# Kernel optimization log

Measured on AMD Instinct MI355X. Metric: run time of the kernel, lower is better.

The kernel has to match this reference:

```python
import jax, jax.numpy as jnp
import numpy as np

EPS = 1e-8
N_NODES = 100000
N_EDGES = 3200000
S_IN, V_IN = 128, 16
S_OUT, V_OUT = 128, 16
HID = 16          # bottleneck=1 -> max(V_IN, V_OUT)
FRAME_C = 3       # scalarization_vectorization_output_dim
MERGED = HID + S_IN + FRAME_C * 3  # 153


def safe_norm(x, axis):
    return jnp.sqrt(jnp.sum(x * x, axis=axis) + EPS)


def setup_inputs() -> dict:
    key = jax.random.key(0)
    ks = jax.random.split(key, 12)
    scalar_rep = jax.random.normal(ks[0], (N_NODES, S_IN), dtype=jnp.float32)
    vector_rep = jax.random.normal(ks[1], (N_NODES, V_IN, 3), dtype=jnp.float32)
    frames = jax.random.normal(ks[2], (N_EDGES, 3, 3), dtype=jnp.float32)
    edge_index = jax.random.randint(ks[3], (2, N_EDGES), 0, N_NODES, dtype=jnp.int64)
    s = 0.05
    W_down = jax.random.normal(ks[4], (HID, V_IN), dtype=jnp.float32) * s
    W_frames = jax.random.normal(ks[5], (FRAME_C, V_IN), dtype=jnp.float32) * s
    W_scalar = jax.random.normal(ks[6], (S_OUT, MERGED), dtype=jnp.float32) * s
    b_scalar = jnp.zeros((S_OUT,), dtype=jnp.float32)
    W_up = jax.random.normal(ks[7], (V_OUT, HID), dtype=jnp.float32) * s
    W_gate = jax.random.normal(ks[8], (V_OUT, S_OUT), dtype=jnp.float32) * s
    b_gate = jnp.zeros((V_OUT,), dtype=jnp.float32)
    return {"scalar_rep": scalar_rep, "vector_rep": vector_rep, "frames": frames,
            "W_down": W_down, "W_frames": W_frames, "W_scalar": W_scalar,
            "b_scalar": b_scalar, "W_up": W_up, "W_gate": W_gate, "b_gate": b_gate,
            "edge_index": edge_index}


def reference(scalar_rep, vector_rep, frames, W_down, W_frames, W_scalar,
              b_scalar, W_up, W_gate, b_gate, edge_index):
    N = scalar_rep.shape[0]
    row = edge_index[0]
    # vector branch: [N, V, 3] -> [N, 3, V]
    v_pre = jnp.swapaxes(vector_rep, -1, -2)
    vh = jnp.einsum('ntv,hv->nth', v_pre, W_down)          # [N, 3, H]
    vnorm = safe_norm(vh, axis=-2)                          # [N, H]
    vdf = jnp.einsum('ntv,fv->ntf', v_pre, W_frames)        # [N, 3, F=3]
    # scalarize: gather per-edge, frame matmul over spatial dim, scatter-mean
    m = jnp.einsum('est,etf->esf', frames, vdf[row])        # [E, 3(s), 3(f)]
    local = jnp.swapaxes(m, -1, -2).reshape(m.shape[0], 9)  # [E, 9] (f, s) order
    sums = jax.ops.segment_sum(local, row, num_segments=N)
    cnt = jax.ops.segment_sum(jnp.ones((local.shape[0],), dtype=local.dtype),
                              row, num_segments=N)
    scalar_hidden = sums / jnp.maximum(cnt, 1.0)[:, None]   # [N, 9]
    merged = jnp.concatenate([scalar_rep, vnorm, scalar_hidden], axis=-1)  # [N, 153]
    s_out = merged @ W_scalar.T + b_scalar                  # [N, S_OUT]
    # vectorize with sigmoid gate
    v_up = jnp.einsum('nth,vh->ntv', vh, W_up)              # [N, 3, V_OUT]
    v_rep = jnp.swapaxes(v_up, -1, -2)                       # [N, V_OUT, 3]
    gate = jax.nn.silu(s_out) @ W_gate.T + b_gate            # [N, V_OUT]
    v_final = v_rep * jax.nn.sigmoid(gate)[..., None]
    s_final = jax.nn.silu(s_out)
    return s_final, v_final
```

## Files before the change

kernel.cpp:

```cpp
#include <hip/hip_runtime.h>
#include <hip/hip_bf16.h>
#include <math.h>

#define N_NODES 100000
#define N_EDGES 3200000
#define NB 16
#define EPSV 1e-8f

#define NBUCK 782
#define NCHUNK 1280
#define CHUNK_E 2500

#define CE 256
#define RS 264

typedef __attribute__((ext_vector_type(8))) short short8;
typedef __attribute__((ext_vector_type(4))) float f32x4;

static __device__ __forceinline__ unsigned short f2bf(float x) {
  union { float f; unsigned int u; } c; c.f = x;
  unsigned int r = c.u + 0x7fff + ((c.u >> 16) & 1);
  return (unsigned short)(r >> 16);
}

__global__ __launch_bounds__(256) void hist_kernel(const int* __restrict__ row,
                                                   unsigned short* __restrict__ hist,
                                                   unsigned short* __restrict__ lscan) {
  __shared__ int lh[NBUCK];
  __shared__ int wtot[4];
  for (int i = threadIdx.x; i < NBUCK; i += 256) lh[i] = 0;
  __syncthreads();
  const int c = blockIdx.x;
  const int e1 = c * CHUNK_E + CHUNK_E;
  for (int e = c * CHUNK_E + threadIdx.x; e < e1; e += 256)
    atomicAdd(&lh[row[e] >> 7], 1);
  __syncthreads();
  const int t = threadIdx.x, lane = t & 63, wid = t >> 6;
  const int b0 = t * 4;
  int h[4];
#pragma unroll
  for (int j = 0; j < 4; ++j) h[j] = (b0 + j < NBUCK) ? lh[b0 + j] : 0;
  int s = h[0] + h[1] + h[2] + h[3];
  int incl = s;
#pragma unroll
  for (int d = 1; d < 64; d <<= 1) {
    int o = __shfl_up(incl, d);
    if (lane >= d) incl += o;
  }
  if (lane == 63) wtot[wid] = incl;
  __syncthreads();
  int pre = incl - s;
  for (int w = 0; w < wid; ++w) pre += wtot[w];
#pragma unroll
  for (int j = 0; j < 4; ++j) {
    if (b0 + j < NBUCK) {
      hist [(size_t)c * NBUCK + b0 + j] = (unsigned short)h[j];
      lscan[(size_t)c * NBUCK + b0 + j] = (unsigned short)pre;
    }
    pre += h[j];
  }
}

__global__ __launch_bounds__(256) void scanc_kernel(const unsigned short* __restrict__ hist,
                                                    unsigned short* __restrict__ cscan,
                                                    int* __restrict__ total) {
  __shared__ int s[2][NCHUNK];
  const int b = blockIdx.x;
  const int t = threadIdx.x;
  for (int i = t; i < NCHUNK; i += 256) s[0][i] = hist[(size_t)i * NBUCK + b];
  __syncthreads();
  int src = 0;
  for (int off = 1; off < NCHUNK; off <<= 1) {
    int dst = src ^ 1;
    for (int i = t; i < NCHUNK; i += 256)
      s[dst][i] = s[src][i] + ((i >= off) ? s[src][i - off] : 0);
    __syncthreads();
    src = dst;
  }
  for (int i = t; i < NCHUNK; i += 256)
    cscan[(size_t)i * NBUCK + b] = (unsigned short)((i == 0) ? 0 : s[src][i - 1]);
  if (t == 0) total[b] = s[src][NCHUNK - 1];
}

__global__ __launch_bounds__(256) void scanb_kernel(const int* __restrict__ total,
                                                    int* __restrict__ base) {
  __shared__ int s[2][1024];
  const int t = threadIdx.x;
  for (int i = t; i < 1024; i += 256) s[0][i] = (i < NBUCK) ? total[i] : 0;
  __syncthreads();
  int src = 0;
  for (int off = 1; off < 1024; off <<= 1) {
    int dst = src ^ 1;
    for (int i = t; i < 1024; i += 256)
      s[dst][i] = s[src][i] + ((i >= off) ? s[src][i - off] : 0);
    __syncthreads();
    src = dst;
  }
  for (int i = t; i <= NBUCK; i += 256) base[i] = (i == 0) ? 0 : s[src][i - 1];
}

__global__ __launch_bounds__(512) void scatter_kernel(const int* __restrict__ row,
                                                      const unsigned short* __restrict__ lscan,
                                                      const unsigned short* __restrict__ cscan,
                                                      const int* __restrict__ base,
                                                      const float* __restrict__ frames,
                                                      unsigned int* __restrict__ payload) {
  __shared__ unsigned int sbuf[CHUNK_E * 5];
  __shared__ int lstart[NBUCK], loff[NBUCK], runG[NBUCK];
  const int c = blockIdx.x, tid = threadIdx.x;

  for (int i = tid; i < NBUCK; i += 512) {
    int st = (int)lscan[(size_t)c * NBUCK + i];
    lstart[i] = st;
    loff[i] = st;
    runG[i] = base[i] + (int)cscan[(size_t)c * NBUCK + i];
  }
  __syncthreads();

  const int e0 = c * CHUNK_E;
  for (int e = e0 + tid; e < e0 + CHUNK_E; e += 512) {
    int r = row[e];
    const float* f = frames + (size_t)e * 9;
    unsigned int w0 = f2bf(f[0]) | ((unsigned)f2bf(f[1]) << 16);
    unsigned int w1 = f2bf(f[2]) | ((unsigned)f2bf(f[3]) << 16);
    unsigned int w2 = f2bf(f[4]) | ((unsigned)f2bf(f[5]) << 16);
    unsigned int w3 = f2bf(f[6]) | ((unsigned)f2bf(f[7]) << 16);
    unsigned int w4 = f2bf(f[8]) | ((unsigned)(r & 127) << 16);
    int p = atomicAdd(&loff[r >> 7], 1);
    unsigned int* d = sbuf + p * 5;
    d[0] = w0; d[1] = w1; d[2] = w2; d[3] = w3; d[4] = w4;
  }
  __syncthreads();

  const int grp = tid >> 4, gl = tid & 15;
  for (int b = grp; b < NBUCK; b += 32) {
    int ls = lstart[b] * 5;
    int n5 = (loff[b] - lstart[b]) * 5;
    size_t gs = (size_t)runG[b] * 5;
    for (int d = gl; d < n5; d += 16)
      payload[gs + d] = sbuf[ls + d];
  }
}

__global__ __launch_bounds__(256) void reduce_kernel(const unsigned int* __restrict__ payload,
                                                     const int* __restrict__ base,
                                                     float* __restrict__ acc) {
  __shared__ unsigned short stg[2][16][RS];
  const int tid = threadIdx.x;
  const int b = blockIdx.x;
  const int wid = tid >> 6, lane = tid & 63;
  const int lr = lane & 15, lk = lane >> 4;

  for (int i = tid; i < RS; i += 256) {
    stg[0][9][i] = 0x3F80; stg[1][9][i] = 0x3F80;
  }

  const int p0 = base[b], p1 = base[b + 1];
  const int nch = (p1 - p0 + CE - 1) / CE;
  const int s0 = wid * 2;
  const unsigned na = (unsigned)((s0 << 4) | lr);
  const unsigned nbod = (unsigned)(((s0 + 1) << 4) | lr);

  f32x4 c0 = {0.f, 0.f, 0.f, 0.f};
  f32x4 c1 = {0.f, 0.f, 0.f, 0.f};

  auto STAGE = [&](int c, int buf) {
    int p = p0 + c * CE + tid;
    if (p < p1) {
      const unsigned int* s = payload + (size_t)p * 5;
      unsigned int w0 = s[0], w1 = s[1], w2 = s[2], w3 = s[3], w4 = s[4];
      stg[buf][0][tid] = (unsigned short)w0;
      stg[buf][1][tid] = (unsigned short)(w0 >> 16);
      stg[buf][2][tid] = (unsigned short)w1;
      stg[buf][3][tid] = (unsigned short)(w1 >> 16);
      stg[buf][4][tid] = (unsigned short)w2;
      stg[buf][5][tid] = (unsigned short)(w2 >> 16);
      stg[buf][6][tid] = (unsigned short)w3;
      stg[buf][7][tid] = (unsigned short)(w3 >> 16);
      stg[buf][8][tid] = (unsigned short)w4;
      stg[buf][10][tid] = (unsigned short)(w4 >> 16);
    } else {
#pragma unroll
      for (int k = 0; k < 9; ++k) stg[buf][k][tid] = 0;
      stg[buf][10][tid] = 0xFFFF;
    }
  };

  auto COMP = [&](int buf) {
#pragma unroll
    for (int g = 0; g < 8; ++g) {
      short8 bf = *(const short8*)&stg[buf][lr][g * 32 + lk * 8];
      short8 nv = *(const short8*)&stg[buf][10][g * 32 + lk * 8];
      short8 a0, a1;
#pragma unroll
      for (int j = 0; j < 8; ++j) {
        unsigned nid = (unsigned short)nv[j];
        a0[j] = (short)((nid == na)   ? 0x3F80 : 0);
        a1[j] = (short)((nid == nbod) ? 0x3F80 : 0);
      }
      c0 = __builtin_amdgcn_mfma_f32_16x16x32_bf16(a0, bf, c0, 0, 0, 0);
      c1 = __builtin_amdgcn_mfma_f32_16x16x32_bf16(a1, bf, c1, 0, 0, 0);
    }
  };

  if (nch > 0) {
    STAGE(0, 0);
    __syncthreads();
    for (int c = 0; c < nch; ++c) {
      if (c + 1 < nch) STAGE(c + 1, (c + 1) & 1);
      COMP(c & 1);
      __syncthreads();
    }
  }
  const int n0 = b << 7;
  if (lr < 10) {
#pragma unroll
    for (int j = 0; j < 4; ++j) {
      int r = lk * 4 + j;
      int x0 = n0 + s0 * 16 + r;
      int x1 = n0 + (s0 + 1) * 16 + r;
      if (x0 < N_NODES) acc[(size_t)x0 * 10 + lr] = c0[j];
      if (x1 < N_NODES) acc[(size_t)x1 * 10 + lr] = c1[j];
    }
  }
}

__global__ __launch_bounds__(256) void prep_kernel(const float* __restrict__ Ws,
                                                   const float* __restrict__ Wg,
                                                   unsigned short* __restrict__ wsWs,
                                                   unsigned short* __restrict__ wsWg) {
  int idx = blockIdx.x * 256 + threadIdx.x;
  if (idx < 8 * 5 * 512) {
    int j = idx & 7, l = (idx >> 3) & 63, t = idx >> 9;
    int nt = t / 5, kk = t - nt * 5;
    int o = nt * 16 + (l & 15);
    int m = kk * 32 + ((l >> 4) << 3) + j;
    wsWs[idx] = (m < 153) ? f2bf(Ws[o * 153 + m]) : (unsigned short)0;
  }
  if (idx < 4 * 512) {
    int j = idx & 7, l = (idx >> 3) & 63, kk = idx >> 9;
    int v = l & 15;
    int m = kk * 32 + ((l >> 4) << 3) + j;
    wsWg[idx] = f2bf(Wg[v * 128 + m]);
  }
}

__global__ __launch_bounds__(256, 4) void node_kernel(
    const float* __restrict__ scalar_rep,
    const float* __restrict__ vrep,
    const float* __restrict__ Wd,
    const float* __restrict__ Wf,
    const float* __restrict__ bs,
    const float* __restrict__ Wu,
    const float* __restrict__ bg,
    const unsigned short* __restrict__ wsWs,
    const unsigned short* __restrict__ wsWg,
    const float* __restrict__ acc,
    float* __restrict__ out_s,
    float* __restrict__ out_v) {
  __shared__ alignas(16) unsigned short s_mergedb[16 * 168];
  __shared__ alignas(16) unsigned short s_sfb[16 * 136];
  __shared__ float s_vrep[16][48];
  __shared__ float s_vh[16][48];
  __shared__ float s_vdf[16][12];
  __shared__ float s_gate[16][16];
  __shared__ float s_WdT[256], s_WuT[256], s_Wf[48], s_bs[128], s_bg[16];

  const int tid = threadIdx.x;
  {
    int a = tid >> 4, b = tid & 15;
    s_WdT[b * 16 + a] = Wd[tid];
    s_WuT[b * 16 + a] = Wu[tid];
  }
  if (tid < 48) s_Wf[tid] = Wf[tid];
  if (tid < 128) s_bs[tid] = bs[tid];
  if (tid < 16) s_bg[tid] = bg[tid];
  if (tid < 240) {
    int r = tid / 15, c = 153 + tid % 15;
    s_mergedb[r * 168 + c] = 0;
  }

  const int i4 = tid >> 4, j4 = tid & 15;
  const int wid = tid >> 6, lane = tid & 63;
  const int lr = lane & 15, lk = lane >> 4;

  const float4* scalar4 = (const float4*)scalar_rep;
  const float4* vrep4 = (const float4*)vrep;

  for (int g = blockIdx.x; g < N_NODES / NB; g += gridDim.x) {
    const int n0 = g * NB;
    __syncthreads();
    for (int idx = tid; idx < 512; idx += 256) {
      float4 v = scalar4[(size_t)n0 * 32 + idx];
      int r = idx >> 5, c4 = idx & 31;
      unsigned short* d = s_mergedb + r * 168 + c4 * 4;
      d[0] = f2bf(v.x); d[1] = f2bf(v.y); d[2] = f2bf(v.z); d[3] = f2bf(v.w);
    }
    for (int idx = tid; idx < 192; idx += 256)
      ((float4*)s_vrep)[idx] = vrep4[(size_t)n0 * 12 + idx];
    __syncthreads();
    {
      float a0 = 0.f, a1 = 0.f, a2 = 0.f;
#pragma unroll
      for (int v = 0; v < 16; ++v) {
        float w = s_WdT[v * 16 + j4];
        a0 += s_vrep[i4][v * 3 + 0] * w;
        a1 += s_vrep[i4][v * 3 + 1] * w;
        a2 += s_vrep[i4][v * 3 + 2] * w;
      }
      s_vh[i4][j4]      = a0;
      s_vh[i4][16 + j4] = a1;
      s_vh[i4][32 + j4] = a2;
      s_mergedb[i4 * 168 + 128 + j4] = f2bf(sqrtf(a0 * a0 + a1 * a1 + a2 * a2 + EPSV));
    }
    if (j4 < 9) {
      int t = j4 / 3, f = j4 - t * 3;
      float a = 0.f;
#pragma unroll
      for (int v = 0; v < 16; ++v)
        a += s_vrep[i4][v * 3 + t] * s_Wf[f * 16 + v];
      s_vdf[i4][j4] = a;
    }
    __syncthreads();
    if (j4 < 9) {
      int f = j4 / 3, s = j4 - f * 3;
      const float* a = acc + (size_t)(n0 + i4) * 10;
      float c = fmaxf(a[9], 1.0f);
      float sum = a[s * 3 + 0] * s_vdf[i4][0 + f] +
                  a[s * 3 + 1] * s_vdf[i4][3 + f] +
                  a[s * 3 + 2] * s_vdf[i4][6 + f];
      s_mergedb[i4 * 168 + 144 + j4] = f2bf(sum / c);
    }
    __syncthreads();
    {
      const int nt0 = wid * 2;
      short8 afrag[5];
#pragma unroll
      for (int kk = 0; kk < 5; ++kk)
        afrag[kk] = *(const short8*)(s_mergedb + lr * 168 + kk * 32 + lk * 8);
      float b0v = s_bs[nt0 * 16 + lr], b1v = s_bs[nt0 * 16 + 16 + lr];
      f32x4 acc0 = {b0v, b0v, b0v, b0v};
      f32x4 acc1 = {b1v, b1v, b1v, b1v};
#pragma unroll
      for (int kk = 0; kk < 5; ++kk) {
        short8 bf0 = *(const short8*)(wsWs + (((nt0 * 5 + kk) << 6) + lane) * 8);
        short8 bf1 = *(const short8*)(wsWs + ((((nt0 + 1) * 5 + kk) << 6) + lane) * 8);
        acc0 = __builtin_amdgcn_mfma_f32_16x16x32_bf16(afrag[kk], bf0, acc0, 0, 0, 0);
        acc1 = __builtin_amdgcn_mfma_f32_16x16x32_bf16(afrag[kk], bf1, acc1, 0, 0, 0);
      }
#pragma unroll
      for (int j = 0; j < 4; ++j) {
        int node = lk * 4 + j;
        float x0 = acc0[j];
        float sf0 = x0 / (1.0f + __expf(-x0));
        out_s[(size_t)(n0 + node) * 128 + nt0 * 16 + lr] = sf0;
        s_sfb[node * 136 + nt0 * 16 + lr] = f2bf(sf0);
        float x1 = acc1[j];
        float sf1 = x1 / (1.0f + __expf(-x1));
        out_s[(size_t)(n0 + node) * 128 + nt0 * 16 + 16 + lr] = sf1;
        s_sfb[node * 136 + nt0 * 16 + 16 + lr] = f2bf(sf1);
      }
    }
    __syncthreads();
    if (wid == 0) {
      float gb = s_bg[lr];
      f32x4 gacc = {gb, gb, gb, gb};
#pragma unroll
      for (int kk = 0; kk < 4; ++kk) {
        short8 ga = *(const short8*)(s_sfb + lr * 136 + kk * 32 + lk * 8);
        short8 gw = *(const short8*)(wsWg + (((kk << 6) + lane) * 8));
        gacc = __builtin_amdgcn_mfma_f32_16x16x32_bf16(ga, gw, gacc, 0, 0, 0);
      }
#pragma unroll
      for (int j = 0; j < 4; ++j) {
        int node = lk * 4 + j;
        s_gate[node][lr] = 1.0f / (1.0f + __expf(-gacc[j]));
      }
    }
    __syncthreads();
    {
      float b0 = 0.f, b1 = 0.f, b2 = 0.f;
#pragma unroll
      for (int h = 0; h < 16; ++h) {
        float w = s_WuT[h * 16 + j4];
        b0 += s_vh[i4][h]      * w;
        b1 += s_vh[i4][16 + h] * w;
        b2 += s_vh[i4][32 + h] * w;
      }
      float gt = s_gate[i4][j4];
      size_t basep = (size_t)(n0 + i4) * 48 + (size_t)j4 * 3;
      out_v[basep + 0] = b0 * gt;
      out_v[basep + 1] = b1 * gt;
      out_v[basep + 2] = b2 * gt;
    }
  }
}

extern "C" void kernel_launch(void* const* d_in, const int* in_sizes, int n_in,
                              void* d_out, int out_size, void* d_ws, size_t ws_size,
                              hipStream_t stream) {
  const float* scalar_rep = (const float*)d_in[0];
  const float* vector_rep = (const float*)d_in[1];
  const float* frames     = (const float*)d_in[2];
  const float* W_down     = (const float*)d_in[3];
  const float* W_frames   = (const float*)d_in[4];
  const float* W_scalar   = (const float*)d_in[5];
  const float* b_scalar   = (const float*)d_in[6];
  const float* W_up       = (const float*)d_in[7];
  const float* W_gate     = (const float*)d_in[8];
  const float* b_gate     = (const float*)d_in[9];
  const int*   edge_index = (const int*)d_in[10];

  float* out = (float*)d_out;

  unsigned short* hist  = (unsigned short*)d_ws;
  unsigned short* lscan = hist  + (size_t)NCHUNK * NBUCK;
  unsigned short* cscan = lscan + (size_t)NCHUNK * NBUCK;
  int*   total   = (int*)(cscan + (size_t)NCHUNK * NBUCK);
  int*   base    = total + 800;
  unsigned int* payload = (unsigned int*)(base + 800);
  float* acc     = (float*)(payload + 16000000);
  unsigned short* wsWs = (unsigned short*)(acc + 1000000);
  unsigned short* wsWg = wsWs + 20480;

  prep_kernel   <<<80,     256, 0, stream>>>(W_scalar, W_gate, wsWs, wsWg);
  hist_kernel   <<<NCHUNK, 256, 0, stream>>>(edge_index, hist, lscan);
  scanc_kernel  <<<NBUCK,  256, 0, stream>>>(hist, cscan, total);
  scanb_kernel  <<<1,      256, 0, stream>>>(total, base);
  scatter_kernel<<<NCHUNK, 512, 0, stream>>>(edge_index, lscan, cscan, base,
                                             frames, payload);
  reduce_kernel <<<NBUCK,  256, 0, stream>>>(payload, base, acc);

  node_kernel<<<768, 256, 0, stream>>>(
      scalar_rep, vector_rep, W_down, W_frames, b_scalar,
      W_up, b_gate, wsWs, wsWg, acc,
      out, out + (size_t)N_NODES * 128);
}
```

Before: 198.7 us.

## Stage frames through LDS with coalesced uint4 loads and shrink scatter chunks

The scatter kernel now loads each half-chunk of frames with coalesced 16-byte vector loads, converts them to bf16 and stages them in shared memory before packing per-edge payloads. This replaces the earlier strided 9-float-per-thread global reads. The chunk count rises to 2000 with 1600 edges each, which shrinks shared memory per block so more blocks can be resident. The column scan now writes back into the hist buffer, dropping the separate cscan array. The trade-off is extra barriers, a second shared-memory staging pass, and larger histogram/scan arrays because there are more chunks.

Measured after the change: 213.1 us. 1.07x slower.

```diff
diff --git a/kernel.cpp b/kernel.cpp
--- a/kernel.cpp
+++ b/kernel.cpp
@@ -8,8 +8,9 @@
 #define EPSV 1e-8f
 
 #define NBUCK 782
-#define NCHUNK 1280
-#define CHUNK_E 2500
+#define NCHUNK 2000
+#define CHUNK_E 1600
+#define HALF_E 800
 
 #define CE 256
 #define RS 264
@@ -20,6 +21,10 @@
 static __device__ __forceinline__ unsigned short f2bf(float x) {
   union { float f; unsigned int u; } c; c.f = x;
   unsigned int r = c.u + 0x7fff + ((c.u >> 16) & 1);
+  return (unsigned short)(r >> 16);
+}
+static __device__ __forceinline__ unsigned short f2bf_bits(unsigned int u) {
+  unsigned int r = u + 0x7fff + ((u >> 16) & 1);
   return (unsigned short)(r >> 16);
 }
 
@@ -61,8 +66,7 @@
   }
 }
 
-__global__ __launch_bounds__(256) void scanc_kernel(const unsigned short* __restrict__ hist,
-                                                    unsigned short* __restrict__ cscan,
+__global__ __launch_bounds__(256) void scanc_kernel(unsigned short* __restrict__ hist,
                                                     int* __restrict__ total) {
   __shared__ int s[2][NCHUNK];
   const int b = blockIdx.x;
@@ -78,7 +82,7 @@
     src = dst;
   }
   for (int i = t; i < NCHUNK; i += 256)
-    cscan[(size_t)i * NBUCK + b] = (unsigned short)((i == 0) ? 0 : s[src][i - 1]);
+    hist[(size_t)i * NBUCK + b] = (unsigned short)((i == 0) ? 0 : s[src][i - 1]);
   if (t == 0) total[b] = s[src][NCHUNK - 1];
 }
 
@@ -106,6 +110,7 @@
                                                       const float* __restrict__ frames,
                                                       unsigned int* __restrict__ payload) {
   __shared__ unsigned int sbuf[CHUNK_E * 5];
+  __shared__ unsigned int rawb[HALF_E * 9 / 2];
   __shared__ int lstart[NBUCK], loff[NBUCK], runG[NBUCK];
   const int c = blockIdx.x, tid = threadIdx.x;
 
@@ -115,20 +120,31 @@
     loff[i] = st;
     runG[i] = base[i] + (int)cscan[(size_t)c * NBUCK + i];
   }
-  __syncthreads();
-
+
+  const unsigned short* raw16 = (const unsigned short*)rawb;
   const int e0 = c * CHUNK_E;
-  for (int e = e0 + tid; e < e0 + CHUNK_E; e += 512) {
-    int r = row[e];
-    const float* f = frames + (size_t)e * 9;
-    unsigned int w0 = f2bf(f[0]) | ((unsigned)f2bf(f[1]) << 16);
-    unsigned int w1 = f2bf(f[2]) | ((unsigned)f2bf(f[3]) << 16);
-    unsigned int w2 = f2bf(f[4]) | ((unsigned)f2bf(f[5]) << 16);
-    unsigned int w3 = f2bf(f[6]) | ((unsigned)f2bf(f[7]) << 16);
-    unsigned int w4 = f2bf(f[8]) | ((unsigned)(r & 127) << 16);
-    int p = atomicAdd(&loff[r >> 7], 1);
-    unsigned int* d = sbuf + p * 5;
-    d[0] = w0; d[1] = w1; d[2] = w2; d[3] = w3; d[4] = w4;
+  for (int h = 0; h < 2; ++h) {
+    __syncthreads();
+    const uint4* fr4 = (const uint4*)(frames + (size_t)(e0 + h * HALF_E) * 9);
+    for (int i = tid; i < HALF_E * 9 / 4; i += 512) {
+      uint4 q = fr4[i];
+      rawb[i * 2]     = f2bf_bits(q.x) | ((unsigned)f2bf_bits(q.y) << 16);
+      rawb[i * 2 + 1] = f2bf_bits(q.z) | ((unsigned)f2bf_bits(q.w) << 16);
+    }
+    __syncthreads();
+    for (int le = tid; le < HALF_E; le += 512) {
+      int e = e0 + h * HALF_E + le;
+      int r = row[e];
+      int bix = le * 9;
+      unsigned w0 = raw16[bix + 0] | ((unsigned)raw16[bix + 1] << 16);
+      unsigned w1 = raw16[bix + 2] | ((unsigned)raw16[bix + 3] << 16);
+      unsigned w2 = raw16[bix + 4] | ((unsigned)raw16[bix + 5] << 16);
+      unsigned w3 = raw16[bix + 6] | ((unsigned)raw16[bix + 7] << 16);
+      unsigned w4 = raw16[bix + 8] | ((unsigned)(r & 127) << 16);
+      int p = atomicAdd(&loff[r >> 7], 1);
+      unsigned int* d = sbuf + p * 5;
+      d[0] = w0; d[1] = w1; d[2] = w2; d[3] = w3; d[4] = w4;
+    }
   }
   __syncthreads();
 
@@ -415,8 +431,7 @@
 
   unsigned short* hist  = (unsigned short*)d_ws;
   unsigned short* lscan = hist  + (size_t)NCHUNK * NBUCK;
-  unsigned short* cscan = lscan + (size_t)NCHUNK * NBUCK;
-  int*   total   = (int*)(cscan + (size_t)NCHUNK * NBUCK);
+  int*   total   = (int*)(lscan + (size_t)NCHUNK * NBUCK);
   int*   base    = total + 800;
   unsigned int* payload = (unsigned int*)(base + 800);
   float* acc     = (float*)(payload + 16000000);
@@ -425,9 +440,9 @@
 
   prep_kernel   <<<80,     256, 0, stream>>>(W_scalar, W_gate, wsWs, wsWg);
   hist_kernel   <<<NCHUNK, 256, 0, stream>>>(edge_index, hist, lscan);
-  scanc_kernel  <<<NBUCK,  256, 0, stream>>>(hist, cscan, total);
+  scanc_kernel  <<<NBUCK,  256, 0, stream>>>(hist, total);
   scanb_kernel  <<<1,      256, 0, stream>>>(total, base);
-  scatter_kernel<<<NCHUNK, 512, 0, stream>>>(edge_index, lscan, cscan, base,
+  scatter_kernel<<<NCHUNK, 512, 0, stream>>>(edge_index, lscan, hist, base,
                                              frames, payload);
   reduce_kernel <<<NBUCK,  256, 0, stream>>>(payload, base, acc);
 
```
